# Performance work log

Hardware: AMD Instinct MI355X
Metric: run time of the kernel (lower is better)

## Reference

```python
import jax, jax.numpy as jnp
import numpy as np

B, N, D = 8, 2048, 1024
A_STDP, TAU_STDP, W_OFF, T_MAX = 0.9, 0.5, 0.9, 1.0
V_TH, EPS = 1.0, 1e-5


def setup_inputs() -> dict:
    key = jax.random.key(0)
    ks = jax.random.split(key, 6)
    s = 0.02
    inp = {"x": jax.random.normal(ks[0], (B, N, D), dtype=jnp.float32)}
    for i, nm in enumerate(["q", "k", "v"]):
        inp[f"W{nm}"] = jax.random.normal(ks[1 + i], (D, D), dtype=jnp.float32) * s
        inp[f"g{nm}"] = jnp.ones((D,), jnp.float32)
        inp[f"b{nm}"] = jnp.zeros((D,), jnp.float32)
        inp[f"m{nm}"] = jnp.zeros((D,), jnp.float32)
        inp[f"v{nm}"] = jnp.ones((D,), jnp.float32)
    inp["Wo"] = jax.random.normal(ks[4], (D, D), dtype=jnp.float32) * s
    inp["bo"] = jnp.zeros((D,), jnp.float32)
    return inp


def _proj(x, W, g, b, m, v):
    # Linear (no bias) -> BatchNorm1d (inference, running stats) -> LIF first step
    h = x @ W                                     # [B,N,D]
    h = (h - m) * (g * jax.lax.rsqrt(v + EPS)) + b
    # LIF with mem=None: mem = x, spike = sigmoid(4*(mem - v_th))
    return jax.nn.sigmoid(4.0 * (h - V_TH))


def reference(x, Wq, gq, bq, mq, vq, Wk, gk, bk, mk, vk, Wv, gv, bv, mv, vv, Wo, bo):
    Q = _proj(x, Wq, gq, bq, mq, vq)
    K = _proj(x, Wk, gk, bk, mk, vk)
    V = _proj(x, Wv, gv, bv, mv, vv)
    t_Q = T_MAX * (1.0 - Q.mean(axis=-1, keepdims=True))   # [B,N,1]
    t_K = T_MAX * (1.0 - K.mean(axis=-1, keepdims=True))   # [B,N,1]
    delta_t = t_Q - jnp.swapaxes(t_K, 1, 2)                 # [B,N,N]
    f_stdp = A_STDP * jnp.exp(-jnp.abs(delta_t) / TAU_STDP)
    A = jnp.where(delta_t < 0, f_stdp, -f_stdp) + W_OFF     # [B,N,N]
    return (A @ V) @ Wo + bo                                # [B,N,D]
```

## Files before the change

### kernel.cpp

```cpp
#include <hip/hip_runtime.h>

#define B_ 8
#define N_ 2048
#define D_ 1024
#define M_ (B_*N_)
#define SEGS 64
#define EPB (4096/SEGS)
#define CW 256

typedef __attribute__((ext_vector_type(8))) short short8;
typedef __attribute__((ext_vector_type(4))) float floatx4;

__device__ __forceinline__ ushort f2bf(float f) {
  unsigned u = __builtin_bit_cast(unsigned, f);
  return (ushort)((u + 0x7fffu + ((u >> 16) & 1u)) >> 16);
}
__device__ __forceinline__ float bf2f(ushort u) {
  return __builtin_bit_cast(float, ((unsigned)u) << 16);
}
__device__ __forceinline__ void gload16(const void* g, void* l) {
  __builtin_amdgcn_global_load_lds(
      (const __attribute__((address_space(1))) unsigned*)g,
      (__attribute__((address_space(3))) unsigned*)l, 16, 0, 0);
}
__device__ __forceinline__ float sig4(float h) {
  return 1.0f / (1.0f + __expf(4.0f - 4.0f*h));
}

__global__ __launch_bounds__(256) void conv_x_k(const float4* __restrict__ x,
                                                ushort4* __restrict__ o) {
  int i = blockIdx.x * 256 + threadIdx.x;
  float4 f = x[i];
  ushort4 u;
  u.x = f2bf(f.x); u.y = f2bf(f.y); u.z = f2bf(f.z); u.w = f2bf(f.w);
  o[i] = u;
}

__global__ __launch_bounds__(256) void transpose_k(
    const float* __restrict__ Wq, const float* __restrict__ Wk,
    const float* __restrict__ Wv, const float* __restrict__ Wo,
    ushort* __restrict__ W3T, ushort* __restrict__ WoT) {
  __shared__ float tile[32][33];
  int z = blockIdx.z;
  const float* W = (z == 0) ? Wq : (z == 1) ? Wk : (z == 2) ? Wv : Wo;
  ushort* WT = (z < 3) ? (W3T + (size_t)z * D_ * D_) : WoT;
  int tx = threadIdx.x, ty = threadIdx.y;
  int x = blockIdx.x * 32 + tx;
  int y = blockIdx.y * 32 + ty;
#pragma unroll
  for (int j = 0; j < 32; j += 8)
    tile[ty + j][tx] = W[(size_t)(y + j) * D_ + x];
  __syncthreads();
  int x2 = blockIdx.y * 32 + tx;
  int y2 = blockIdx.x * 32 + ty;
#pragma unroll
  for (int j = 0; j < 32; j += 8)
    WT[(size_t)(y2 + j) * D_ + x2] = f2bf(tile[tx][ty + j]);
}

__device__ __forceinline__ void mainloop256(
    const ushort* __restrict__ Ab, const ushort* __restrict__ Bb,
    ushort* __restrict__ As, ushort* __restrict__ Bs, int t,
    floatx4 (&acc)[8][4])
{
  const int lane = t & 63, wid = t >> 6;
  const int quad = lane >> 4, l15 = lane & 15;
  const int wm = wid >> 2, wn = wid & 3;

  int srcO[2], dsto[2];
#pragma unroll
  for (int r = 0; r < 2; r++) {
    int li = r * 512 + t;
    int row = li >> 2, c = li & 3;
    int soff = ((c - (row >> 1)) & 3) * 8;
    srcO[r] = row * D_ + soff;
    dsto[r] = li * 16;
  }

  int offA[8], offB[4];
#pragma unroll
  for (int i = 0; i < 8; i++) {
    int row = wm * 128 + i * 16 + l15;
    offA[i] = row * 32 + ((quad + (row >> 1)) & 3) * 8;
  }
#pragma unroll
  for (int i = 0; i < 4; i++) {
    int row = wn * 64 + i * 16 + l15;
    offB[i] = row * 32 + ((quad + (row >> 1)) & 3) * 8;
  }

#pragma unroll
  for (int pt = 0; pt < 3; pt++) {
#pragma unroll
    for (int r = 0; r < 2; r++)
      gload16(Ab + srcO[r] + pt * 32, (char*)(As + pt * 8192) + dsto[r]);
#pragma unroll
    for (int r = 0; r < 2; r++)
      gload16(Bb + srcO[r] + pt * 32, (char*)(Bs + pt * 8192) + dsto[r]);
  }

  const int NT = D_ / 32;
#pragma unroll 4
  for (int tt = 0; tt < NT; tt++) {
    if (tt < NT - 2)       asm volatile("s_waitcnt vmcnt(8)" ::: "memory");
    else if (tt == NT - 2) asm volatile("s_waitcnt vmcnt(4)" ::: "memory");
    else                   asm volatile("s_waitcnt vmcnt(0)" ::: "memory");
    __builtin_amdgcn_s_barrier();
    const ushort* Asl = As + (tt & 3) * 8192;
    const ushort* Bsl = Bs + (tt & 3) * 8192;
    const bool pf = (tt + 3 < NT);

    short8 af[4], bfr[4];
#pragma unroll
    for (int i = 0; i < 4; i++) af[i] = *(const short8*)(Asl + offA[i]);
#pragma unroll
    for (int i = 0; i < 4; i++) bfr[i] = *(const short8*)(Bsl + offB[i]);
    if (pf) {
      ushort* d = As + ((tt + 3) & 3) * 8192;
#pragma unroll
      for (int r = 0; r < 2; r++)
        gload16(Ab + srcO[r] + (tt + 3) * 32, (char*)d + dsto[r]);
    }
    __builtin_amdgcn_s_barrier();
    __builtin_amdgcn_sched_barrier(0);
    __builtin_amdgcn_s_setprio(1);
#pragma unroll
    for (int tm = 0; tm < 4; tm++)
#pragma unroll
      for (int tn = 0; tn < 4; tn++)
        acc[tm][tn] = __builtin_amdgcn_mfma_f32_16x16x32_bf16(
            af[tm], bfr[tn], acc[tm][tn], 0, 0, 0);
    __builtin_amdgcn_s_setprio(0);

    short8 ag[4];
#pragma unroll
    for (int i = 0; i < 4; i++) ag[i] = *(const short8*)(Asl + offA[4 + i]);
    if (pf) {
      ushort* d = Bs + ((tt + 3) & 3) * 8192;
#pragma unroll
      for (int r = 0; r < 2; r++)
        gload16(Bb + srcO[r] + (tt + 3) * 32, (char*)d + dsto[r]);
    }
    __builtin_amdgcn_s_barrier();
    __builtin_amdgcn_sched_barrier(0);
    __builtin_amdgcn_s_setprio(1);
#pragma unroll
    for (int tm = 0; tm < 4; tm++)
#pragma unroll
      for (int tn = 0; tn < 4; tn++)
        acc[4 + tm][tn] = __builtin_amdgcn_mfma_f32_16x16x32_bf16(
            ag[tm], bfr[tn], acc[4 + tm][tn], 0, 0, 0);
    __builtin_amdgcn_s_setprio(0);
  }
}

__global__ __launch_bounds__(512, 2) void gemm_qkv_k(
    const ushort* __restrict__ A, const ushort* __restrict__ W3T,
    const float* __restrict__ gq, const float* __restrict__ bq,
    const float* __restrict__ mq, const float* __restrict__ vq,
    const float* __restrict__ gk, const float* __restrict__ bk,
    const float* __restrict__ mk, const float* __restrict__ vk,
    const float* __restrict__ gv, const float* __restrict__ bv,
    const float* __restrict__ mv, const float* __restrict__ vv,
    float* __restrict__ rsQ, float* __restrict__ rsK, ushort* __restrict__ Vb)
{
  __shared__ ushort As[4 * 8192];
  __shared__ ushort Bs[4 * 8192];
  const int t = threadIdx.x;
  const int lane = t & 63, wid = t >> 6;
  const int quad = lane >> 4, l15 = lane & 15;
  const int wm = wid >> 2, wn = wid & 3;

  const int lin = blockIdx.x;
  const int xcd = lin & 7, s = lin >> 3;
  const int z = s >> 5;
  const int rem = s & 31;
  const int mg = rem >> 2;
  const int nt = rem & 3;
  const int tileM = (xcd * 8 + mg) * 256;
  const int tileN = nt * 256;

  const float* gg  = (z == 0) ? gq : (z == 1) ? gk : gv;
  const float* bb  = (z == 0) ? bq : (z == 1) ? bk : bv;
  const float* mmn = (z == 0) ? mq : (z == 1) ? mk : mv;
  const float* vvn = (z == 0) ? vq : (z == 1) ? vk : vv;

  float sc[4], sh[4];
#pragma unroll
  for (int tn = 0; tn < 4; tn++) {
    int col = tileN + wn * 64 + tn * 16 + l15;
    float scv = gg[col] * rsqrtf(vvn[col] + 1e-5f);
    sc[tn] = scv;
    sh[tn] = bb[col] - mmn[col] * scv;
  }
  asm volatile("s_waitcnt vmcnt(0)" ::: "memory");

  floatx4 acc[8][4];
#pragma unroll
  for (int i = 0; i < 8; i++)
#pragma unroll
    for (int j = 0; j < 4; j++) acc[i][j] = (floatx4){0.f, 0.f, 0.f, 0.f};

  mainloop256(A + (size_t)tileM * D_,
              W3T + (size_t)z * D_ * D_ + (size_t)tileN * D_,
              As, Bs, t, acc);

  if (z == 2) {
#pragma unroll
    for (int tm = 0; tm < 8; tm++) {
      int row0 = tileM + wm * 128 + tm * 16 + quad * 4;
#pragma unroll
      for (int tn = 0; tn < 4; tn++) {
        int col = tileN + wn * 64 + tn * 16 + l15;
#pragma unroll
        for (int r = 0; r < 4; r++)
          Vb[(size_t)(row0 + r) * D_ + col] =
              f2bf(sig4(acc[tm][tn][r] * sc[tn] + sh[tn]));
      }
    }
  } else {
    float* rowsum = (z == 0) ? rsQ : rsK;
#pragma unroll
    for (int tm = 0; tm < 8; tm++) {
      float rs[4] = {0.f, 0.f, 0.f, 0.f};
#pragma unroll
      for (int tn = 0; tn < 4; tn++)
#pragma unroll
        for (int r = 0; r < 4; r++)
          rs[r] += sig4(acc[tm][tn][r] * sc[tn] + sh[tn]);
#pragma unroll
      for (int off = 1; off < 16; off <<= 1)
#pragma unroll
        for (int r = 0; r < 4; r++)
          rs[r] += __shfl_xor(rs[r], off, 64);
      if (l15 == 0) {
        int row0 = tileM + wm * 128 + tm * 16 + quad * 4;
#pragma unroll
        for (int r = 0; r < 4; r++)
          atomicAdd(&rowsum[row0 + r], rs[r]);
      }
    }
  }
}

__global__ __launch_bounds__(512, 2) void gemm_out_k(
    const ushort* __restrict__ A, const ushort* __restrict__ Bt,
    float* __restrict__ outF, const float* __restrict__ bo)
{
  __shared__ ushort As[4 * 8192];
  __shared__ ushort Bs[4 * 8192];
  const int t = threadIdx.x;
  const int lane = t & 63, wid = t >> 6;
  const int quad = lane >> 4, l15 = lane & 15;
  const int wm = wid >> 2, wn = wid & 3;

  const int lin = blockIdx.x;
  const int xcd = lin & 7, s = lin >> 3;
  const int mg = s >> 2, nt = s & 3;
  const int tileM = (xcd * 8 + mg) * 256;
  const int tileN = nt * 256;

  float bias[4];
#pragma unroll
  for (int tn = 0; tn < 4; tn++)
    bias[tn] = bo[tileN + wn * 64 + tn * 16 + l15];
  asm volatile("s_waitcnt vmcnt(0)" ::: "memory");

  floatx4 acc[8][4];
#pragma unroll
  for (int i = 0; i < 8; i++)
#pragma unroll
    for (int j = 0; j < 4; j++) acc[i][j] = (floatx4){0.f, 0.f, 0.f, 0.f};

  mainloop256(A + (size_t)tileM * D_, Bt + (size_t)tileN * D_, As, Bs, t, acc);

#pragma unroll
  for (int tm = 0; tm < 8; tm++) {
    int row0 = tileM + wm * 128 + tm * 16 + quad * 4;
#pragma unroll
    for (int tn = 0; tn < 4; tn++) {
      int col = tileN + wn * 64 + tn * 16 + l15;
#pragma unroll
      for (int r = 0; r < 4; r++)
        outF[(size_t)(row0 + r) * D_ + col] = acc[tm][tn][r] + bias[tn];
    }
  }
}

__global__ __launch_bounds__(256) void rank_events_k(
    const float* __restrict__ rsQ, const float* __restrict__ rsK,
    int* __restrict__ evt_tag, float* __restrict__ evt_wa, float* __restrict__ evt_wd)
{
  __shared__ unsigned long long keys[4096];
  __shared__ int part[256];
  int b = blockIdx.y, chunk = blockIdx.x;
  int t = threadIdx.x;
  for (int i = t; i < 4096; i += 256) {
    float v; unsigned tag;
    if (i < 2048) {
      v = 1.0f - rsQ[b * N_ + i] * (1.0f / 1024.0f);
      tag = (unsigned)i | 0x10000u;
    } else {
      int j = i - 2048;
      v = 1.0f - rsK[b * N_ + j] * (1.0f / 1024.0f);
      tag = (unsigned)j;
    }
    keys[i] = ((unsigned long long)__builtin_bit_cast(unsigned, v) << 32) | tag;
  }
  __syncthreads();
  int e = chunk * 128 + (t & 127);
  int j0 = (t >> 7) * 2048;
  unsigned long long me = keys[e];
  int r = 0;
#pragma unroll 8
  for (int j = 0; j < 2048; j++) r += (keys[j0 + j] < me) ? 1 : 0;
  part[t] = r;
  __syncthreads();
  if (t < 128) {
    int rank = part[t] + part[t + 128];
    unsigned tag = (unsigned)(me & 0x1FFFFu);
    float v = __builtin_bit_cast(float, (unsigned)(me >> 32));
    bool isq = (tag & 0x10000u) != 0;
    int o = b * 4096 + rank;
    evt_tag[o] = (int)tag;
    evt_wa[o] = isq ? expf(-2.0f * v) : expf(2.0f * v);
    evt_wd[o] = isq ? expf(2.0f * v) : expf(-2.0f * v);
  }
}

__global__ __launch_bounds__(256) void seg_tot_k(
    const int* __restrict__ evt_tag, const float* __restrict__ evt_wa,
    const float* __restrict__ evt_wd, const ushort* __restrict__ Vb,
    float* __restrict__ totWA, float* __restrict__ totWD, float* __restrict__ totP)
{
  __shared__ int srow[EPB];
  __shared__ float swa[EPB], swd[EPB], spw[EPB];
  int b = blockIdx.z, seg = blockIdx.y, chunk = blockIdx.x;
  int t = threadIdx.x;
  int e0 = b * 4096 + seg * EPB;
  if (t < EPB) {
    int tg = evt_tag[e0 + t];
    bool isk = !(tg & 0x10000);
    srow[t] = isk ? (tg & 0xFFFF) : 0;
    swa[t] = isk ? evt_wa[e0 + t] : 0.f;
    swd[t] = isk ? evt_wd[e0 + t] : 0.f;
    spw[t] = isk ? 1.f : 0.f;
  }
  __syncthreads();
  int c = chunk * 512 + t * 2;
  const ushort* vb = Vb + (size_t)b * N_ * D_ + c;
  float wa0 = 0, wa1 = 0, wd0 = 0, wd1 = 0, p0 = 0, p1 = 0;
#pragma unroll 8
  for (int e = 0; e < EPB; e++) {
    unsigned raw = *(const unsigned*)(vb + (size_t)srow[e] * D_);
    float v0 = bf2f((ushort)(raw & 0xffffu)), v1 = bf2f((ushort)(raw >> 16));
    float wa = swa[e], wd = swd[e], pw = spw[e];
    wa0 += wa * v0; wa1 += wa * v1;
    wd0 += wd * v0; wd1 += wd * v1;
    p0 += pw * v0;  p1 += pw * v1;
  }
  size_t o = ((size_t)b * SEGS + seg) * D_ + c;
  totWA[o] = wa0; totWA[o + 1] = wa1;
  totWD[o] = wd0; totWD[o + 1] = wd1;
  totP[o]  = p0;  totP[o + 1]  = p1;
}

__global__ __launch_bounds__(256) void seg_prefix_k(
    const float* __restrict__ totWA, const float* __restrict__ totWD,
    const float* __restrict__ totP,
    float* __restrict__ preA, float* __restrict__ sufD,
    float* __restrict__ Vsum)
{
  int b = blockIdx.y;
  int c = blockIdx.x * 256 + threadIdx.x;
  size_t base = (size_t)b * SEGS * D_ + c;

  float va[SEGS];
  float psum = 0.f;
#pragma unroll
  for (int s = 0; s < SEGS; s++) {
    va[s] = totWA[base + (size_t)s * D_];
    psum += totP[base + (size_t)s * D_];
  }
  Vsum[b * D_ + c] = psum;
  float a = 0.f;
#pragma unroll
  for (int s = 0; s < SEGS; s++) {
    preA[base + (size_t)s * D_] = a;
    a += va[s];
  }

  float vd[SEGS];
#pragma unroll
  for (int s = 0; s < SEGS; s++)
    vd[s] = totWD[base + (size_t)s * D_];
  float d = 0.f;
#pragma unroll
  for (int s = SEGS - 1; s >= 0; s--) {
    sufD[base + (size_t)s * D_] = d;
    d += vd[s];
  }
}

__global__ __launch_bounds__(256) void scan_one_k(
    const int* __restrict__ evt_tag, const float* __restrict__ evt_wa,
    const float* __restrict__ evt_wd, const ushort* __restrict__ Vb,
    const float* __restrict__ preA, const float* __restrict__ sufD,
    const float* __restrict__ totWD, const float* __restrict__ Vsum,
    ushort* __restrict__ AVb)
{
  __shared__ ushort Vt[EPB * CW];
  __shared__ int sisq[EPB], sidx[EPB], srow[EPB];
  __shared__ float skwa[EPB], skwd[EPB], sqwa[EPB], sqwd[EPB];
  int b = blockIdx.z, seg = blockIdx.y, chunk = blockIdx.x;
  int t = threadIdx.x;
  int e0 = b * 4096 + seg * EPB;
  if (t < EPB) {
    int tg = evt_tag[e0 + t];
    bool isq = (tg & 0x10000) != 0;
    float wa = evt_wa[e0 + t], wd = evt_wd[e0 + t];
    sisq[t] = isq; sidx[t] = isq ? (tg & 0xFFFF) : 0;
    srow[t] = isq ? 0 : (tg & 0xFFFF);
    skwa[t] = isq ? 0.f : wa;  sqwa[t] = wa;
    skwd[t] = isq ? 0.f : wd;  sqwd[t] = wd;
  }
  __syncthreads();
  int c0 = chunk * CW;
  const ushort* vbase = Vb + (size_t)b * N_ * D_ + c0;
#pragma unroll
  for (int r = 0; r < 8; r++) {
    int li = r * 256 + t;
    int e = li >> 5, ch = li & 31;
    gload16(vbase + (size_t)srow[e] * D_ + ch * 8, (char*)Vt + li * 16);
  }
  __syncthreads();

  int cth = c0 + t;
  size_t po = ((size_t)b * SEGS + seg) * D_ + cth;
  float sA   = preA[po];
  float sD0  = sufD[po] + totWD[po];
  float voff = 0.9f * Vsum[b * D_ + cth];
  float sDacc = 0.f;
  ushort* AVbrow = AVb + (size_t)b * N_ * D_ + cth;

#pragma unroll 4
  for (int e = 0; e < EPB; e++) {
    float v = bf2f(Vt[e * CW + t]);
    if (sisq[e]) {
      float out = voff + 0.9f * (sqwd[e] * (sD0 - sDacc) - sqwa[e] * sA);
      AVbrow[(size_t)sidx[e] * D_] = f2bf(out);
    }
    sA    += skwa[e] * v;
    sDacc += skwd[e] * v;
  }
}

extern "C" void kernel_launch(void* const* d_in, const int* in_sizes, int n_in,
                              void* d_out, int out_size, void* d_ws, size_t ws_size,
                              hipStream_t stream) {
  (void)in_sizes; (void)n_in; (void)out_size; (void)ws_size;
  const float* x  = (const float*)d_in[0];
  const float* Wq = (const float*)d_in[1];
  const float* gq = (const float*)d_in[2];
  const float* bq = (const float*)d_in[3];
  const float* mq = (const float*)d_in[4];
  const float* vq = (const float*)d_in[5];
  const float* Wk = (const float*)d_in[6];
  const float* gk = (const float*)d_in[7];
  const float* bk = (const float*)d_in[8];
  const float* mk = (const float*)d_in[9];
  const float* vk = (const float*)d_in[10];
  const float* Wv = (const float*)d_in[11];
  const float* gv = (const float*)d_in[12];
  const float* bv = (const float*)d_in[13];
  const float* mv = (const float*)d_in[14];
  const float* vv = (const float*)d_in[15];
  const float* Wo = (const float*)d_in[16];
  const float* bo = (const float*)d_in[17];

  char* p = (char*)d_ws;
  auto alloc = [&](size_t n) { char* r = p; p += n; return r; };
  ushort* x16  = (ushort*)alloc((size_t)M_ * D_ * 2);
  ushort* Vb   = (ushort*)alloc((size_t)M_ * D_ * 2);
  ushort* AVb  = (ushort*)alloc((size_t)M_ * D_ * 2);
  ushort* W3T  = (ushort*)alloc((size_t)3 * D_ * D_ * 2);
  ushort* WoT  = (ushort*)alloc((size_t)D_ * D_ * 2);
  float*  rsQ  = (float*)alloc((size_t)M_ * 4);
  float*  rsK  = (float*)alloc((size_t)M_ * 4);
  int*    evt_tag = (int*)alloc((size_t)B_ * 4096 * 4);
  float*  evt_wa  = (float*)alloc((size_t)B_ * 4096 * 4);
  float*  evt_wd  = (float*)alloc((size_t)B_ * 4096 * 4);
  float*  totWA   = (float*)alloc((size_t)B_ * SEGS * D_ * 4);
  float*  totWD   = (float*)alloc((size_t)B_ * SEGS * D_ * 4);
  float*  totP    = (float*)alloc((size_t)B_ * SEGS * D_ * 4);
  float*  preA    = (float*)alloc((size_t)B_ * SEGS * D_ * 4);
  float*  sufD    = (float*)alloc((size_t)B_ * SEGS * D_ * 4);
  float*  VsumW   = (float*)alloc((size_t)B_ * D_ * 4);

  hipMemsetAsync(rsQ, 0, (size_t)2 * M_ * 4, stream);

  conv_x_k<<<(M_ * D_) / 1024, 256, 0, stream>>>((const float4*)x, (ushort4*)x16);
  dim3 tb(32, 8), tg(32, 32, 4);
  transpose_k<<<tg, tb, 0, stream>>>(Wq, Wk, Wv, Wo, W3T, WoT);

  gemm_qkv_k<<<768, 512, 0, stream>>>(x16, W3T, gq, bq, mq, vq,
                                      gk, bk, mk, vk, gv, bv, mv, vv,
                                      rsQ, rsK, Vb);

  rank_events_k<<<dim3(32, B_), 256, 0, stream>>>(rsQ, rsK, evt_tag, evt_wa, evt_wd);

  seg_tot_k<<<dim3(2, SEGS, B_), 256, 0, stream>>>(evt_tag, evt_wa, evt_wd, Vb,
                                                   totWA, totWD, totP);
  seg_prefix_k<<<dim3(D_ / 256, B_), 256, 0, stream>>>(totWA, totWD, totP,
                                                       preA, sufD, VsumW);
  scan_one_k<<<dim3(D_ / CW, SEGS, B_), 256, 0, stream>>>(
      evt_tag, evt_wa, evt_wd, Vb, preA, sufD, totWD, VsumW, AVb);

  gemm_out_k<<<256, 512, 0, stream>>>(AVb, WoT, (float*)d_out, bo);
}
```

Measured before the change: 397.0 us.

## Switch GEMM mainloop to double-buffered LDS and raise occupancy to four blocks

Replaces the 4-stage LDS ring (prefetch depth 3, split barriers and explicit vmcnt waits) with a simple 2-stage double buffer using __syncthreads, halving shared memory per block. Launch bounds go from 2 to 4 blocks per CU for the QKV and output GEMMs, BN/bias parameter loads move after the mainloop, and seg_prefix reuses one register array. The intent is more resident waves to hide latency in place of a deep software pipeline. The risk is register spills under the tighter bound (256 fp32 accumulators per lane must fit in a smaller budget) and less prefetch depth.

```diff
diff --git a/kernel.cpp b/kernel.cpp
--- a/kernel.cpp
+++ b/kernel.cpp
@@ -90,39 +90,31 @@
   }
 
 #pragma unroll
-  for (int pt = 0; pt < 3; pt++) {
-#pragma unroll
-    for (int r = 0; r < 2; r++)
-      gload16(Ab + srcO[r] + pt * 32, (char*)(As + pt * 8192) + dsto[r]);
-#pragma unroll
-    for (int r = 0; r < 2; r++)
-      gload16(Bb + srcO[r] + pt * 32, (char*)(Bs + pt * 8192) + dsto[r]);
+  for (int r = 0; r < 2; r++) {
+    gload16(Ab + srcO[r], (char*)As + dsto[r]);
+    gload16(Bb + srcO[r], (char*)Bs + dsto[r]);
   }
 
   const int NT = D_ / 32;
-#pragma unroll 4
+#pragma unroll 2
   for (int tt = 0; tt < NT; tt++) {
-    if (tt < NT - 2)       asm volatile("s_waitcnt vmcnt(8)" ::: "memory");
-    else if (tt == NT - 2) asm volatile("s_waitcnt vmcnt(4)" ::: "memory");
-    else                   asm volatile("s_waitcnt vmcnt(0)" ::: "memory");
-    __builtin_amdgcn_s_barrier();
-    const ushort* Asl = As + (tt & 3) * 8192;
-    const ushort* Bsl = Bs + (tt & 3) * 8192;
-    const bool pf = (tt + 3 < NT);
-
-    short8 af[4], bfr[4];
+    __syncthreads();
+    const ushort* Asl = As + (tt & 1) * 8192;
+    const ushort* Bsl = Bs + (tt & 1) * 8192;
+    if (tt + 1 < NT) {
+      ushort* dA = As + ((tt + 1) & 1) * 8192;
+      ushort* dB = Bs + ((tt + 1) & 1) * 8192;
+#pragma unroll
+      for (int r = 0; r < 2; r++) {
+        gload16(Ab + srcO[r] + (tt + 1) * 32, (char*)dA + dsto[r]);
+        gload16(Bb + srcO[r] + (tt + 1) * 32, (char*)dB + dsto[r]);
+      }
+    }
+    short8 af[4], bfr[4], ag[4];
 #pragma unroll
     for (int i = 0; i < 4; i++) af[i] = *(const short8*)(Asl + offA[i]);
 #pragma unroll
     for (int i = 0; i < 4; i++) bfr[i] = *(const short8*)(Bsl + offB[i]);
-    if (pf) {
-      ushort* d = As + ((tt + 3) & 3) * 8192;
-#pragma unroll
-      for (int r = 0; r < 2; r++)
-        gload16(Ab + srcO[r] + (tt + 3) * 32, (char*)d + dsto[r]);
-    }
-    __builtin_amdgcn_s_barrier();
-    __builtin_amdgcn_sched_barrier(0);
     __builtin_amdgcn_s_setprio(1);
 #pragma unroll
     for (int tm = 0; tm < 4; tm++)
@@ -131,18 +123,8 @@
         acc[tm][tn] = __builtin_amdgcn_mfma_f32_16x16x32_bf16(
             af[tm], bfr[tn], acc[tm][tn], 0, 0, 0);
     __builtin_amdgcn_s_setprio(0);
-
-    short8 ag[4];
 #pragma unroll
     for (int i = 0; i < 4; i++) ag[i] = *(const short8*)(Asl + offA[4 + i]);
-    if (pf) {
-      ushort* d = Bs + ((tt + 3) & 3) * 8192;
-#pragma unroll
-      for (int r = 0; r < 2; r++)
-        gload16(Bb + srcO[r] + (tt + 3) * 32, (char*)d + dsto[r]);
-    }
-    __builtin_amdgcn_s_barrier();
-    __builtin_amdgcn_sched_barrier(0);
     __builtin_amdgcn_s_setprio(1);
 #pragma unroll
     for (int tm = 0; tm < 4; tm++)
@@ -154,7 +136,7 @@
   }
 }
 
-__global__ __launch_bounds__(512, 2) void gemm_qkv_k(
+__global__ __launch_bounds__(512, 4) void gemm_qkv_k(
     const ushort* __restrict__ A, const ushort* __restrict__ W3T,
     const float* __restrict__ gq, const float* __restrict__ bq,
     const float* __restrict__ mq, const float* __restrict__ vq,
@@ -164,8 +146,8 @@
     const float* __restrict__ mv, const float* __restrict__ vv,
     float* __restrict__ rsQ, float* __restrict__ rsK, ushort* __restrict__ Vb)
 {
-  __shared__ ushort As[4 * 8192];
-  __shared__ ushort Bs[4 * 8192];
+  __shared__ ushort As[2 * 8192];
+  __shared__ ushort Bs[2 * 8192];
   const int t = threadIdx.x;
   const int lane = t & 63, wid = t >> 6;
   const int quad = lane >> 4, l15 = lane & 15;
@@ -180,11 +162,20 @@
   const int tileM = (xcd * 8 + mg) * 256;
   const int tileN = nt * 256;
 
+  floatx4 acc[8][4];
+#pragma unroll
+  for (int i = 0; i < 8; i++)
+#pragma unroll
+    for (int j = 0; j < 4; j++) acc[i][j] = (floatx4){0.f, 0.f, 0.f, 0.f};
+
+  mainloop256(A + (size_t)tileM * D_,
+              W3T + (size_t)z * D_ * D_ + (size_t)tileN * D_,
+              As, Bs, t, acc);
+
   const float* gg  = (z == 0) ? gq : (z == 1) ? gk : gv;
   const float* bb  = (z == 0) ? bq : (z == 1) ? bk : bv;
   const float* mmn = (z == 0) ? mq : (z == 1) ? mk : mv;
   const float* vvn = (z == 0) ? vq : (z == 1) ? vk : vv;
-
   float sc[4], sh[4];
 #pragma unroll
   for (int tn = 0; tn < 4; tn++) {
@@ -193,17 +184,6 @@
     sc[tn] = scv;
     sh[tn] = bb[col] - mmn[col] * scv;
   }
-  asm volatile("s_waitcnt vmcnt(0)" ::: "memory");
-
-  floatx4 acc[8][4];
-#pragma unroll
-  for (int i = 0; i < 8; i++)
-#pragma unroll
-    for (int j = 0; j < 4; j++) acc[i][j] = (floatx4){0.f, 0.f, 0.f, 0.f};
-
-  mainloop256(A + (size_t)tileM * D_,
-              W3T + (size_t)z * D_ * D_ + (size_t)tileN * D_,
-              As, Bs, t, acc);
 
   if (z == 2) {
 #pragma unroll
@@ -243,12 +223,12 @@
   }
 }
 
-__global__ __launch_bounds__(512, 2) void gemm_out_k(
+__global__ __launch_bounds__(512, 4) void gemm_out_k(
     const ushort* __restrict__ A, const ushort* __restrict__ Bt,
     float* __restrict__ outF, const float* __restrict__ bo)
 {
-  __shared__ ushort As[4 * 8192];
-  __shared__ ushort Bs[4 * 8192];
+  __shared__ ushort As[2 * 8192];
+  __shared__ ushort Bs[2 * 8192];
   const int t = threadIdx.x;
   const int lane = t & 63, wid = t >> 6;
   const int quad = lane >> 4, l15 = lane & 15;
@@ -260,12 +240,6 @@
   const int tileM = (xcd * 8 + mg) * 256;
   const int tileN = nt * 256;
 
-  float bias[4];
-#pragma unroll
-  for (int tn = 0; tn < 4; tn++)
-    bias[tn] = bo[tileN + wn * 64 + tn * 16 + l15];
-  asm volatile("s_waitcnt vmcnt(0)" ::: "memory");
-
   floatx4 acc[8][4];
 #pragma unroll
   for (int i = 0; i < 8; i++)
@@ -275,14 +249,15 @@
   mainloop256(A + (size_t)tileM * D_, Bt + (size_t)tileN * D_, As, Bs, t, acc);
 
 #pragma unroll
-  for (int tm = 0; tm < 8; tm++) {
-    int row0 = tileM + wm * 128 + tm * 16 + quad * 4;
-#pragma unroll
-    for (int tn = 0; tn < 4; tn++) {
-      int col = tileN + wn * 64 + tn * 16 + l15;
+  for (int tn = 0; tn < 4; tn++) {
+    int col = tileN + wn * 64 + tn * 16 + l15;
+    float bias = bo[col];
+#pragma unroll
+    for (int tm = 0; tm < 8; tm++) {
+      int row0 = tileM + wm * 128 + tm * 16 + quad * 4;
 #pragma unroll
       for (int r = 0; r < 4; r++)
-        outF[(size_t)(row0 + r) * D_ + col] = acc[tm][tn][r] + bias[tn];
+        outF[(size_t)(row0 + r) * D_ + col] = acc[tm][tn][r] + bias;
     }
   }
 }
@@ -376,13 +351,9 @@
   size_t base = (size_t)b * SEGS * D_ + c;
 
   float va[SEGS];
-  float psum = 0.f;
-#pragma unroll
-  for (int s = 0; s < SEGS; s++) {
+#pragma unroll
+  for (int s = 0; s < SEGS; s++)
     va[s] = totWA[base + (size_t)s * D_];
-    psum += totP[base + (size_t)s * D_];
-  }
-  Vsum[b * D_ + c] = psum;
   float a = 0.f;
 #pragma unroll
   for (int s = 0; s < SEGS; s++) {
@@ -390,16 +361,21 @@
     a += va[s];
   }
 
-  float vd[SEGS];
 #pragma unroll
   for (int s = 0; s < SEGS; s++)
-    vd[s] = totWD[base + (size_t)s * D_];
+    va[s] = totWD[base + (size_t)s * D_];
   float d = 0.f;
 #pragma unroll
   for (int s = SEGS - 1; s >= 0; s--) {
     sufD[base + (size_t)s * D_] = d;
-    d += vd[s];
-  }
+    d += va[s];
+  }
+
+  float psum = 0.f;
+#pragma unroll
+  for (int s = 0; s < SEGS; s++)
+    psum += totP[base + (size_t)s * D_];
+  Vsum[b * D_ + c] = psum;
 }
 
 __global__ __launch_bounds__(256) void scan_one_k(
```

Result: slower. 1.583 ms (+298.8%).
